# Performance work log

Hardware: AMD Instinct MI355X
Metric: run time of the kernel (lower is better)

Reference implementation:

```python
import jax, jax.numpy as jnp
import numpy as np

B, L, D = 2, 2048, 2048
H, KV, HD = 16, 4, 64  # query heads, kv heads, head_dim
EPS = 1e-6
ROPE_BASE = 10000.0


def setup_inputs() -> dict:
    key = jax.random.key(0)
    k0, k1, k2 = jax.random.split(key, 3)
    x = jax.random.normal(k0, (B, L, D), dtype=jnp.float32)
    W_qkv = jax.random.normal(k1, ((H + 2 * KV) * HD, D), dtype=jnp.float32) * 0.02
    W_out = jax.random.normal(k2, (D, H * HD), dtype=jnp.float32) * 0.02
    q_norm_w = jnp.ones((HD,), dtype=jnp.float32)
    k_norm_w = jnp.ones((HD,), dtype=jnp.float32)
    # causal additive mask (forward's optional `mask` arg)
    mask = jnp.triu(jnp.full((L, L), -1e9, dtype=jnp.float32), k=1)
    return {"x": x, "W_qkv": W_qkv, "W_out": W_out,
            "q_norm_w": q_norm_w, "k_norm_w": k_norm_w, "mask": mask}


def _rms_norm(x, w):
    # normalize over last (head) dim
    var = jnp.mean(x * x, axis=-1, keepdims=True)
    return x * jax.lax.rsqrt(var + EPS) * w


def _rope(x):
    # x: [B, nH, L, HD]; non-traditional (rotate-half) RoPE, offset=0
    half = HD // 2
    freqs = ROPE_BASE ** (-jnp.arange(0, HD, 2, dtype=jnp.float32) / HD)  # [half]
    theta = jnp.arange(L, dtype=jnp.float32)[:, None] * freqs[None, :]    # [L, half]
    cos, sin = jnp.cos(theta), jnp.sin(theta)
    x1, x2 = x[..., :half], x[..., half:]
    return jnp.concatenate([x1 * cos - x2 * sin, x1 * sin + x2 * cos], axis=-1)


def reference(x, W_qkv, W_out, q_norm_w, k_norm_w, mask):
    # fused QKV projection
    qkv = jnp.einsum("bld,ed->ble", x, W_qkv)                       # [B,L,(H+2KV)*HD]
    qkv = qkv.reshape(B, L, H + 2 * KV, HD).transpose(0, 2, 1, 3)   # [B,nH,L,HD]
    q, k, v = jnp.split(qkv, [H, H + KV], axis=1)
    # per-head QK RMSNorm + RoPE
    q = _rope(_rms_norm(q, q_norm_w))
    k = _rope(_rms_norm(k, k_norm_w))
    # GQA: repeat kv heads to match query heads
    rep = H // KV
    k = jnp.repeat(k, rep, axis=1)
    v = jnp.repeat(v, rep, axis=1)
    scale = HD ** -0.5
    scores = jnp.einsum("bhqd,bhkd->bhqk", q, k) * scale + mask      # [B,H,L,L]
    attn = jax.nn.softmax(scores, axis=-1)
    out = jnp.einsum("bhqk,bhkd->bhqd", attn, v)                     # [B,H,L,HD]
    out = out.transpose(0, 2, 1, 3).reshape(B, L, H * HD)
    return jnp.einsum("ble,de->bld", out, W_out)                     # [B,L,D]
```

## Files before the change

kernel.cpp:

```cpp
#include <hip/hip_runtime.h>
#include <hip/hip_bf16.h>


typedef __bf16 bf16;
typedef bf16 bf16x8 __attribute__((ext_vector_type(8)));
typedef bf16 bf16x4 __attribute__((ext_vector_type(4)));
typedef float f32x4 __attribute__((ext_vector_type(4)));

#define L_SEQ 2048
#define NQH 16
#define NKVH 4

typedef __attribute__((address_space(3))) void lds_void;
typedef const __attribute__((address_space(1))) void glb_void;
__device__ __forceinline__ void async_ld16(const void* g, void* l) {
  __builtin_amdgcn_global_load_lds((glb_void*)g, (lds_void*)l, 16, 0, 0);
}

__global__ __launch_bounds__(256) void cast_bf16(const float* __restrict__ in,
                                                 bf16* __restrict__ out, int n) {
  int i = (blockIdx.x * 256 + threadIdx.x) * 4;
  if (i < n) {
    float4 v = *(const float4*)&in[i];
    bf16x4 o;
    o[0] = (bf16)v.x; o[1] = (bf16)v.y; o[2] = (bf16)v.z; o[3] = (bf16)v.w;
    *(bf16x4*)&out[i] = o;
  }
}

__global__ __launch_bounds__(256)
void gemm_bt(const bf16* __restrict__ A, const bf16* __restrict__ B,
             float* __restrict__ C, int M, int N, int K) {
  __shared__ bf16 As[128 * 32];
  __shared__ bf16 Bs[128 * 32];
  const int tid = threadIdx.x;
  const int lane = tid & 63, w = tid >> 6;
  const int lq = lane & 15, g = lane >> 4;
  const int wr = w >> 1, wc = w & 1;
  const int bx = blockIdx.x, by = blockIdx.y;

  const bf16* gA[2];
  const bf16* gB[2];
  bf16* ldsA[2];
  bf16* ldsB[2];
#pragma unroll
  for (int c = 0; c < 2; ++c) {
    int slot = c * 256 + tid;
    int row = slot >> 2, ch = slot & 3;
    int sch = ch ^ ((row >> 1) & 3);
    gA[c] = &A[(size_t)(by * 128 + row) * K + sch * 8];
    gB[c] = &B[(size_t)(bx * 128 + row) * K + sch * 8];
    int wbase = (c * 256 + w * 64) * 8;
    ldsA[c] = &As[wbase];
    ldsB[c] = &Bs[wbase];
  }

  f32x4 acc[4][4] = {};

  const int nk = K >> 5;
  for (int kt = 0; kt < nk; ++kt) {
#pragma unroll
    for (int c = 0; c < 2; ++c) {
      async_ld16(gA[c] + kt * 32, ldsA[c]);
      async_ld16(gB[c] + kt * 32, ldsB[c]);
    }
    __syncthreads();
    bf16x8 af[4], bfr[4];
#pragma unroll
    for (int i = 0; i < 4; ++i) {
      int ra = wr * 64 + i * 16 + lq;
      af[i] = *(const bf16x8*)&As[ra * 32 + (g ^ ((ra >> 1) & 3)) * 8];
      int rb = wc * 64 + i * 16 + lq;
      bfr[i] = *(const bf16x8*)&Bs[rb * 32 + (g ^ ((rb >> 1) & 3)) * 8];
    }
#pragma unroll
    for (int i = 0; i < 4; ++i)
#pragma unroll
      for (int j = 0; j < 4; ++j)
        acc[i][j] = __builtin_amdgcn_mfma_f32_16x16x32_bf16(af[i], bfr[j], acc[i][j], 0, 0, 0);
    __syncthreads();
  }
#pragma unroll
  for (int i = 0; i < 4; ++i)
#pragma unroll
    for (int j = 0; j < 4; ++j) {
      int row = by * 128 + wr * 64 + i * 16 + g * 4;
      int col = bx * 128 + wc * 64 + j * 16 + lq;
#pragma unroll
      for (int r = 0; r < 4; ++r) C[(size_t)(row + r) * N + col] = acc[i][j][r];
    }
}

__global__ __launch_bounds__(256)
void norm_rope(const float* __restrict__ qkv, const float* __restrict__ qw,
               const float* __restrict__ kw, bf16* __restrict__ Qb,
               bf16* __restrict__ Kb, bf16* __restrict__ Vb) {
  const int bl = blockIdx.x;
  const int b = bl >> 11, l = bl & (L_SEQ - 1);
  const int w = threadIdx.x >> 6, lane = threadIdx.x & 63;
  const int i = lane & 31;
  float freq = exp2f(-(float)i * 0.41524101186280154f);
  float theta = (float)l * freq;
  float sn, cs;
  sincosf(theta, &sn, &cs);
  float qwl = qw[lane], kwl = kw[lane];

  for (int h = w; h < 24; h += 4) {
    float v = qkv[(size_t)bl * 1536 + h * 64 + lane];
    if (h < 20) {
      float ss = v * v;
#pragma unroll
      for (int off = 32; off; off >>= 1) ss += __shfl_xor(ss, off);
      float rs = rsqrtf(ss * (1.f / 64.f) + 1e-6f);
      float wt = (h < 16) ? qwl : kwl;
      float y = v * rs * wt;
      float part = __shfl_xor(y, 32);
      float out = (lane < 32) ? (y * cs - part * sn) : (part * sn + y * cs);
      if (h < 16)
        Qb[((size_t)(b * NQH + h) * L_SEQ + l) * 64 + lane] = (bf16)(out * 0.125f);
      else
        Kb[((size_t)(b * NKVH + (h - 16)) * L_SEQ + l) * 64 + lane] = (bf16)out;
    } else {
      Vb[((size_t)(b * NKVH + (h - 20)) * L_SEQ + l) * 64 + lane] = (bf16)v;
    }
  }
}

__global__ __launch_bounds__(256)
void transpose_v(const bf16* __restrict__ Vb, bf16* __restrict__ Vt) {
  __shared__ bf16 T[64 * 66];
  const int bk = blockIdx.y;
  const int l0 = blockIdx.x * 64;
  const int t = threadIdx.x;
  const bf16* src = Vb + (size_t)bk * L_SEQ * 64;
#pragma unroll
  for (int c = 0; c < 2; ++c) {
    int idx = c * 256 + t;
    int row = idx >> 3, ch = idx & 7;
    bf16x8 v = *(const bf16x8*)&src[(size_t)(l0 + row) * 64 + ch * 8];
#pragma unroll
    for (int j = 0; j < 8; ++j) T[(ch * 8 + j) * 66 + row] = v[j];
  }
  __syncthreads();
  bf16* dst = Vt + (size_t)bk * 64 * L_SEQ;
#pragma unroll
  for (int c = 0; c < 2; ++c) {
    int idx = c * 256 + t;
    int d = idx >> 3, ch = idx & 7;
    bf16x8 v;
#pragma unroll
    for (int j = 0; j < 8; ++j) v[j] = T[d * 66 + ch * 8 + j];
    *(bf16x8*)&dst[(size_t)d * L_SEQ + l0 + ch * 8] = v;
  }
}

__global__ __launch_bounds__(256)
void attn(const bf16* __restrict__ Qb, const bf16* __restrict__ Kb,
          const bf16* __restrict__ Vt, bf16* __restrict__ Ao) {
  const int pair = blockIdx.x;
  const int bh = blockIdx.y;
  const int b = bh >> 4, h = bh & 15, kv = h >> 2;
  const int tid = threadIdx.x;
  const int w = tid >> 6, lane = tid & 63;
  const int lq = lane & 15, g = lane >> 4;

  __shared__ bf16 Ks[64][64];
  __shared__ bf16 Vs[64][64];
  __shared__ bf16 Plds[4][16][72];

  const bf16* Qp = Qb + (size_t)(b * NQH + h) * L_SEQ * 64;
  const bf16* Kp = Kb + (size_t)(b * NKVH + kv) * L_SEQ * 64;
  const bf16* Vp = Vt + (size_t)(b * NKVH + kv) * 64 * L_SEQ;

  const int sr0 = tid >> 3, sc = tid & 7;
  const int sr1 = sr0 + 32;
  const int swc0 = (sc ^ (sr0 & 7)) * 8;
  bf16x8 rk0, rk1, rv0, rv1;

  auto load_tile = [&](int k0) {
    rk0 = *(const bf16x8*)&Kp[(size_t)(k0 + sr0) * 64 + sc * 8];
    rk1 = *(const bf16x8*)&Kp[(size_t)(k0 + sr1) * 64 + sc * 8];
    rv0 = *(const bf16x8*)&Vp[(size_t)sr0 * L_SEQ + k0 + sc * 8];
    rv1 = *(const bf16x8*)&Vp[(size_t)sr1 * L_SEQ + k0 + sc * 8];
  };
  auto write_tile = [&]() {
    *(bf16x8*)&Ks[sr0][swc0] = rk0;
    *(bf16x8*)&Ks[sr1][swc0] = rk1;
    *(bf16x8*)&Vs[sr0][swc0] = rv0;
    *(bf16x8*)&Vs[sr1][swc0] = rv1;
  };

  const float L2E = 1.4426950408889634f;

  for (int half = 0; half < 2; ++half) {
    const int qblk = half ? (31 - pair) : pair;
    const int qr0 = qblk * 64 + w * 16;
    const int qg = qr0 + lq;

    bf16x8 qf[2];
    qf[0] = *(const bf16x8*)&Qp[(qr0 + lq) * 64 + g * 8];
    qf[1] = *(const bf16x8*)&Qp[(qr0 + lq) * 64 + 32 + g * 8];

    f32x4 o[4] = {};
    float m = -1e30f, lsum = 0.f;

    const int nkt = qblk + 1;
    load_tile(0);
    __syncthreads();
    write_tile();
    __syncthreads();

    for (int kt = 0; kt < nkt; ++kt) {
      const int k0 = kt * 64;
      const bool diag = (kt == nkt - 1);
      if (kt + 1 < nkt) load_tile(k0 + 64);

      f32x4 s[4] = {};
#pragma unroll
      for (int ks = 0; ks < 4; ++ks) {
        if (!diag || ks <= w) {
          const int row = ks * 16 + lq, sw = lq & 7;
          bf16x8 kf0 = *(const bf16x8*)&Ks[row][(g ^ sw) * 8];
          bf16x8 kf1 = *(const bf16x8*)&Ks[row][((g + 4) ^ sw) * 8];
          s[ks] = __builtin_amdgcn_mfma_f32_16x16x32_bf16(kf0, qf[0], s[ks], 0, 0, 0);
          s[ks] = __builtin_amdgcn_mfma_f32_16x16x32_bf16(kf1, qf[1], s[ks], 0, 0, 0);
        }
      }
      if (diag) {
#pragma unroll
        for (int ks = 0; ks < 4; ++ks)
#pragma unroll
          for (int r = 0; r < 4; ++r)
            if (k0 + ks * 16 + g * 4 + r > qg) s[ks][r] = -1e30f;
      }
      float tmax = -1e30f;
#pragma unroll
      for (int ks = 0; ks < 4; ++ks)
#pragma unroll
        for (int r = 0; r < 4; ++r) tmax = fmaxf(tmax, s[ks][r]);
      tmax = fmaxf(tmax, __shfl_xor(tmax, 16));
      tmax = fmaxf(tmax, __shfl_xor(tmax, 32));
      float mnew = fmaxf(m, tmax);
      float alpha = exp2f((m - mnew) * L2E);
      m = mnew;
      float rsum = 0.f;
#pragma unroll
      for (int ks = 0; ks < 4; ++ks) {
        bf16x4 p;
#pragma unroll
        for (int r = 0; r < 4; ++r) {
          float pv = exp2f((s[ks][r] - mnew) * L2E);
          rsum += pv;
          p[r] = (bf16)pv;
        }
        *(bf16x4*)&Plds[w][lq][ks * 16 + g * 4] = p;
      }
      rsum += __shfl_xor(rsum, 16);
      rsum += __shfl_xor(rsum, 32);
      lsum = lsum * alpha + rsum;

      float ar[4];
#pragma unroll
      for (int r = 0; r < 4; ++r) ar[r] = __shfl(alpha, (lane & 48) | (g * 4 + r));
#pragma unroll
      for (int dt = 0; dt < 4; ++dt)
#pragma unroll
        for (int r = 0; r < 4; ++r) o[dt][r] *= ar[r];

      bf16x8 pf0 = *(const bf16x8*)&Plds[w][lq][g * 8];
      bf16x8 pf1 = *(const bf16x8*)&Plds[w][lq][32 + g * 8];
#pragma unroll
      for (int dt = 0; dt < 4; ++dt) {
        const int row = dt * 16 + lq, sw = lq & 7;
        bf16x8 vf0 = *(const bf16x8*)&Vs[row][(g ^ sw) * 8];
        o[dt] = __builtin_amdgcn_mfma_f32_16x16x32_bf16(pf0, vf0, o[dt], 0, 0, 0);
        if (!diag || w >= 2) {
          bf16x8 vf1 = *(const bf16x8*)&Vs[row][((g + 4) ^ sw) * 8];
          o[dt] = __builtin_amdgcn_mfma_f32_16x16x32_bf16(pf1, vf1, o[dt], 0, 0, 0);
        }
      }

      if (kt + 1 < nkt) {
        __syncthreads();
        write_tile();
        __syncthreads();
      }
    }

    float linv = 1.f / lsum;
#pragma unroll
    for (int r = 0; r < 4; ++r) {
      float li = __shfl(linv, (lane & 48) | (g * 4 + r));
      int row = b * L_SEQ + qr0 + g * 4 + r;
#pragma unroll
      for (int dt = 0; dt < 4; ++dt)
        Ao[(size_t)row * 1024 + h * 64 + dt * 16 + lq] = (bf16)(o[dt][r] * li);
    }
  }
}

extern "C" void kernel_launch(void* const* d_in, const int* in_sizes, int n_in,
                              void* d_out, int out_size, void* d_ws, size_t ws_size,
                              hipStream_t stream) {
  const float* x = (const float*)d_in[0];
  const float* Wqkv = (const float*)d_in[1];
  const float* Wout = (const float*)d_in[2];
  const float* qw = (const float*)d_in[3];
  const float* kw = (const float*)d_in[4];
  float* out = (float*)d_out;

  char* ws = (char*)d_ws;
  size_t off = 0;
  auto alloc = [&](size_t bytes) {
    void* p = ws + off;
    off = (off + bytes + 255) & ~(size_t)255;
    return p;
  };
  bf16* xb = (bf16*)alloc(8388608ull * 2);
  bf16* wqb = (bf16*)alloc(3145728ull * 2);
  bf16* wob = (bf16*)alloc(2097152ull * 2);
  float* qkv = (float*)alloc(4096ull * 1536 * 4);
  bf16* Qb = (bf16*)alloc(4194304ull * 2);
  bf16* Kb = (bf16*)alloc(1048576ull * 2);
  bf16* Vb = (bf16*)alloc(1048576ull * 2);
  bf16* Vt = (bf16*)alloc(1048576ull * 2);
  bf16* Ao = (bf16*)alloc(4194304ull * 2);

  cast_bf16<<<8192, 256, 0, stream>>>(x, xb, 8388608);
  cast_bf16<<<3072, 256, 0, stream>>>(Wqkv, wqb, 3145728);
  cast_bf16<<<2048, 256, 0, stream>>>(Wout, wob, 2097152);
  gemm_bt<<<dim3(12, 32), 256, 0, stream>>>(xb, wqb, qkv, 4096, 1536, 2048);
  norm_rope<<<4096, 256, 0, stream>>>(qkv, qw, kw, Qb, Kb, Vb);
  transpose_v<<<dim3(32, 8), 256, 0, stream>>>(Vb, Vt);
  attn<<<dim3(16, 32), 256, 0, stream>>>(Qb, Kb, Vt, Ao);
  gemm_bt<<<dim3(16, 32), 256, 0, stream>>>(Ao, wob, out, 4096, 2048, 1024);
}
```

Before: 282.5 us.

## Double-buffer GEMM LDS tiles and template N-tile width for QKV projection

Adds double-buffered LDS staging to the bf16 GEMM so the async global-to-LDS load of the next K tile is issued before the MFMAs on the current tile, removing one barrier per iteration. The kernel is templated on the N tile width, and the QKV projection uses a 64-wide tile so it launches 768 blocks instead of 384, which fills more CUs. Costs are doubled LDS use per block and lower per-block reuse for the narrower tile.

Measured after the change: 271.2 us. 1.04x faster.

```diff
diff --git a/kernel.cpp b/kernel.cpp
--- a/kernel.cpp
+++ b/kernel.cpp
@@ -28,11 +28,15 @@
   }
 }
 
+template <int BN>
 __global__ __launch_bounds__(256)
 void gemm_bt(const bf16* __restrict__ A, const bf16* __restrict__ B,
              float* __restrict__ C, int M, int N, int K) {
-  __shared__ bf16 As[128 * 32];
-  __shared__ bf16 Bs[128 * 32];
+  constexpr int ASZ = 128 * 32, BSZ = BN * 32;
+  constexpr int BI = BN / 64;
+  constexpr int NJ = BN / 32;
+  __shared__ bf16 As[2 * ASZ];
+  __shared__ bf16 Bs[2 * BSZ];
   const int tid = threadIdx.x;
   const int lane = tid & 63, w = tid >> 6;
   const int lq = lane & 15, g = lane >> 4;
@@ -40,52 +44,66 @@
   const int bx = blockIdx.x, by = blockIdx.y;
 
   const bf16* gA[2];
-  const bf16* gB[2];
   bf16* ldsA[2];
-  bf16* ldsB[2];
+  const bf16* gB[BI];
+  bf16* ldsB[BI];
 #pragma unroll
   for (int c = 0; c < 2; ++c) {
     int slot = c * 256 + tid;
     int row = slot >> 2, ch = slot & 3;
     int sch = ch ^ ((row >> 1) & 3);
     gA[c] = &A[(size_t)(by * 128 + row) * K + sch * 8];
-    gB[c] = &B[(size_t)(bx * 128 + row) * K + sch * 8];
-    int wbase = (c * 256 + w * 64) * 8;
-    ldsA[c] = &As[wbase];
-    ldsB[c] = &Bs[wbase];
-  }
-
-  f32x4 acc[4][4] = {};
-
+    ldsA[c] = &As[(c * 256 + w * 64) * 8];
+  }
+#pragma unroll
+  for (int c = 0; c < BI; ++c) {
+    int slot = c * 256 + tid;
+    int row = slot >> 2, ch = slot & 3;
+    int sch = ch ^ ((row >> 1) & 3);
+    gB[c] = &B[(size_t)(bx * BN + row) * K + sch * 8];
+    ldsB[c] = &Bs[(c * 256 + w * 64) * 8];
+  }
+
+  auto stage = [&](int kt, int buf) {
+#pragma unroll
+    for (int c = 0; c < 2; ++c) async_ld16(gA[c] + kt * 32, ldsA[c] + buf * ASZ);
+#pragma unroll
+    for (int c = 0; c < BI; ++c) async_ld16(gB[c] + kt * 32, ldsB[c] + buf * BSZ);
+  };
+
+  f32x4 acc[4][NJ] = {};
   const int nk = K >> 5;
+  int cur = 0;
+
+  stage(0, 0);
+  __syncthreads();
   for (int kt = 0; kt < nk; ++kt) {
-#pragma unroll
-    for (int c = 0; c < 2; ++c) {
-      async_ld16(gA[c] + kt * 32, ldsA[c]);
-      async_ld16(gB[c] + kt * 32, ldsB[c]);
-    }
-    __syncthreads();
-    bf16x8 af[4], bfr[4];
+    bf16x8 af[4], bfr[NJ];
 #pragma unroll
     for (int i = 0; i < 4; ++i) {
       int ra = wr * 64 + i * 16 + lq;
-      af[i] = *(const bf16x8*)&As[ra * 32 + (g ^ ((ra >> 1) & 3)) * 8];
-      int rb = wc * 64 + i * 16 + lq;
-      bfr[i] = *(const bf16x8*)&Bs[rb * 32 + (g ^ ((rb >> 1) & 3)) * 8];
-    }
+      af[i] = *(const bf16x8*)&As[cur * ASZ + ra * 32 + (g ^ ((ra >> 1) & 3)) * 8];
+    }
+#pragma unroll
+    for (int j = 0; j < NJ; ++j) {
+      int rb = wc * (BN / 2) + j * 16 + lq;
+      bfr[j] = *(const bf16x8*)&Bs[cur * BSZ + rb * 32 + (g ^ ((rb >> 1) & 3)) * 8];
+    }
+    if (kt + 1 < nk) stage(kt + 1, cur ^ 1);
 #pragma unroll
     for (int i = 0; i < 4; ++i)
 #pragma unroll
-      for (int j = 0; j < 4; ++j)
+      for (int j = 0; j < NJ; ++j)
         acc[i][j] = __builtin_amdgcn_mfma_f32_16x16x32_bf16(af[i], bfr[j], acc[i][j], 0, 0, 0);
     __syncthreads();
+    cur ^= 1;
   }
 #pragma unroll
   for (int i = 0; i < 4; ++i)
 #pragma unroll
-    for (int j = 0; j < 4; ++j) {
+    for (int j = 0; j < NJ; ++j) {
       int row = by * 128 + wr * 64 + i * 16 + g * 4;
-      int col = bx * 128 + wc * 64 + j * 16 + lq;
+      int col = bx * BN + wc * (BN / 2) + j * 16 + lq;
 #pragma unroll
       for (int r = 0; r < 4; ++r) C[(size_t)(row + r) * N + col] = acc[i][j][r];
     }
@@ -329,9 +347,9 @@
   cast_bf16<<<8192, 256, 0, stream>>>(x, xb, 8388608);
   cast_bf16<<<3072, 256, 0, stream>>>(Wqkv, wqb, 3145728);
   cast_bf16<<<2048, 256, 0, stream>>>(Wout, wob, 2097152);
-  gemm_bt<<<dim3(12, 32), 256, 0, stream>>>(xb, wqb, qkv, 4096, 1536, 2048);
+  gemm_bt<64><<<dim3(24, 32), 256, 0, stream>>>(xb, wqb, qkv, 4096, 1536, 2048);
   norm_rope<<<4096, 256, 0, stream>>>(qkv, qw, kw, Qb, Kb, Vb);
   transpose_v<<<dim3(32, 8), 256, 0, stream>>>(Vb, Vt);
   attn<<<dim3(16, 32), 256, 0, stream>>>(Qb, Kb, Vt, Ao);
-  gemm_bt<<<dim3(16, 32), 256, 0, stream>>>(Ao, wob, out, 4096, 2048, 1024);
-}
+  gemm_bt<128><<<dim3(16, 32), 256, 0, stream>>>(Ao, wob, out, 4096, 2048, 1024);
+}
```
